# Kernel optimization log

Hardware: AMD Instinct MI355X
Metric: run time of the kernel (lower is better)

## Reference

```python
import jax, jax.numpy as jnp
import numpy as np

S0 = 192
C = [16, 32, 48, 64, 80]      # nPlanes = m*i, m=16, 5 strides
SL = [192, 96, 48, 24, 12]    # spatial size per level
OFF27 = jnp.asarray(np.stack(np.meshgrid(*([[-1, 0, 1]] * 3), indexing='ij'), -1).reshape(-1, 3), jnp.int32)
OFF8 = jnp.asarray(np.stack(np.meshgrid(*([[0, 1]] * 3), indexing='ij'), -1).reshape(-1, 3), jnp.int32)


def _flat(c, S):
    return (c[..., 0] * S + c[..., 1]) * S + c[..., 2]


def _grid(coords, S):
    g = jnp.full((S * S * S,), -1, jnp.int32)
    return g.at[_flat(coords, S)].set(jnp.arange(coords.shape[0], dtype=jnp.int32))


def _subconv(feat, coords, grid, S, W):
    # submanifold 3x3x3 conv over active sites only; W: [27, a, b]
    nb = coords[:, None, :] + OFF27                      # [N,27,3]
    valid = jnp.all((nb >= 0) & (nb < S), axis=-1)
    idx = grid[_flat(jnp.clip(nb, 0, S - 1), S)]         # [N,27]
    valid = valid & (idx >= 0)
    g = jnp.where(valid[..., None], feat[jnp.maximum(idx, 0)], 0.0)
    return jnp.einsum('nka,kab->nb', g, W)


def _downconv(feat, grid_f, S_f, out_coords, W):
    # kernel-2 stride-2 sparse conv; W: [8, a, b]
    src = out_coords[:, None, :] * 2 + OFF8              # [M,8,3]
    valid = jnp.all(src < S_f, axis=-1)
    idx = grid_f[_flat(src, S_f)]
    valid = valid & (idx >= 0)
    g = jnp.where(valid[..., None], feat[jnp.maximum(idx, 0)], 0.0)
    return jnp.einsum('nka,kab->nb', g, W)


def _bnrelu(x, g, b, eps=1e-4):
    # BatchNormLeakyReLU(leakiness=0) == BN (batch stats over active sites) + ReLU
    mu = jnp.mean(x, 0)
    var = jnp.mean((x - mu) ** 2, 0)
    return jax.nn.relu((x - mu) * jax.lax.rsqrt(var + eps) * g + b)


def _unpool(feat_c, grid_c, S_c, fine_coords, k):
    # UnPooling x k levels: copy coarse parent feature to each fine active site
    return feat_c[grid_c[_flat(fine_coords // (1 << k), S_c)]]


def _selection(scores):
    return (jax.nn.softmax(scores, axis=1)[:, 1:2] > 0.5).astype(scores.dtype)


def _forward(coords, features, w_in, blk_w, blk_g, blk_b, dn_g, dn_b, dn_w,
             ppn1_w, ppn1_sw, ppn2_w, ppn2_sw, ppn3_w, ppn3_pw, ppn3_sw):
    grids = [_grid(coords[l], SL[l]) for l in range(5)]
    x = _subconv(features, coords[0], grids[0], SL[0], w_in)   # input layer
    fmaps = [x]
    for i in range(4):  # encoder levels with residual blocks + downsample
        for r in range(2):
            h = _bnrelu(x, blk_g[i][2 * r], blk_b[i][2 * r])
            h = _subconv(h, coords[i], grids[i], SL[i], blk_w[i][2 * r])
            h = _bnrelu(h, blk_g[i][2 * r + 1], blk_b[i][2 * r + 1])
            h = _subconv(h, coords[i], grids[i], SL[i], blk_w[i][2 * r + 1])
            x = x + h  # ConcatTable(Identity, conv path) + AddTable, a==b
        x = _downconv(_bnrelu(x, dn_g[i], dn_b[i]), grids[i], SL[i], coords[i + 1], dn_w[i])
        fmaps.append(x)
    x = _subconv(x, coords[4], grids[4], SL[4], ppn1_w)
    ppn1_scores = x @ ppn1_sw                                   # 1x1 conv
    att1 = _unpool(_selection(ppn1_scores), grids[4], SL[4], coords[2], 2)
    y = fmaps[2] * att1                                         # Multiply at half_stride
    y = _subconv(y, coords[2], grids[2], SL[2], ppn2_w)
    ppn2_scores = y @ ppn2_sw
    att2 = _unpool(_selection(ppn2_scores), grids[2], SL[2], coords[0], 2)
    z = fmaps[0] * att2
    z = _subconv(z, coords[0], grids[0], SL[0], ppn3_w)
    out0 = jnp.concatenate([z @ ppn3_pw, z @ ppn3_sw], axis=1)
    out1 = jnp.concatenate([coords[4].astype(out0.dtype), ppn1_scores], axis=1)
    out2 = jnp.concatenate([coords[2].astype(out0.dtype), ppn2_scores], axis=1)
    return out0, out1, out2


def _make_coords():
    rng = np.random.RandomState(0)
    c0 = np.unique(rng.randint(0, S0, size=(100000, 3)), axis=0).astype(np.int32)
    cs = [c0]
    for _ in range(4):
        cs.append(np.unique(cs[-1] // 2, axis=0).astype(np.int32))
    return cs


def setup_inputs():
    key = jax.random.key(0)
    ks = iter(jax.random.split(key, 64))
    cs = _make_coords()
    inp = {f'coords{l}': jnp.asarray(cs[l]) for l in range(5)}
    N0 = cs[0].shape[0]
    inp['features'] = jax.random.normal(next(ks), (N0, 1), jnp.float32)

    def w(k, shape, fan):
        return jax.random.normal(k, shape, jnp.float32) * (fan ** -0.5)

    inp['w_in'] = w(next(ks), (27, 1, C[0]), 27)
    for i in range(4):
        inp[f'blk_w{i}'] = w(next(ks), (4, 27, C[i], C[i]), 27 * C[i])
        inp[f'blk_g{i}'] = jnp.ones((4, C[i]), jnp.float32)
        inp[f'blk_b{i}'] = jnp.zeros((4, C[i]), jnp.float32)
        inp[f'dn_g{i}'] = jnp.ones((C[i],), jnp.float32)
        inp[f'dn_b{i}'] = jnp.zeros((C[i],), jnp.float32)
        inp[f'dn_w{i}'] = w(next(ks), (8, C[i], C[i + 1]), 8 * C[i])
    inp['ppn1_w'] = w(next(ks), (27, C[4], C[4]), 27 * C[4])
    inp['ppn1_sw'] = w(next(ks), (C[4], 2), C[4])
    inp['ppn2_w'] = w(next(ks), (27, C[2], C[2]), 27 * C[2])
    inp['ppn2_sw'] = w(next(ks), (C[2], 2), C[2])
    inp['ppn3_w'] = w(next(ks), (27, C[0], C[0]), 27 * C[0])
    inp['ppn3_pw'] = w(next(ks), (C[0], 3), C[0])
    inp['ppn3_sw'] = w(next(ks), (C[0], 2), C[0])
    return inp


def reference(features, w_in,
              blk_w0, blk_g0, blk_b0, dn_g0, dn_b0, dn_w0,
              blk_w1, blk_g1, blk_b1, dn_g1, dn_b1, dn_w1,
              blk_w2, blk_g2, blk_b2, dn_g2, dn_b2, dn_w2,
              blk_w3, blk_g3, blk_b3, dn_g3, dn_b3, dn_w3,
              ppn1_w, ppn1_sw, ppn2_w, ppn2_sw, ppn3_w, ppn3_pw, ppn3_sw,
              coords0, coords1, coords2, coords3, coords4):
    coords = [coords0, coords1, coords2, coords3, coords4]
    return _forward(coords, features, w_in,
                    [blk_w0, blk_w1, blk_w2, blk_w3],
                    [blk_g0, blk_g1, blk_g2, blk_g3],
                    [blk_b0, blk_b1, blk_b2, blk_b3],
                    [dn_g0, dn_g1, dn_g2, dn_g3],
                    [dn_b0, dn_b1, dn_b2, dn_b3],
                    [dn_w0, dn_w1, dn_w2, dn_w3],
                    ppn1_w, ppn1_sw, ppn2_w, ppn2_sw, ppn3_w, ppn3_pw, ppn3_sw)
```

## Files before the change

kernel.cpp:

```cpp
#include <hip/hip_runtime.h>
#include <cstdint>
#include <cstddef>

#define TPB 256

typedef _Float16 f16x8 __attribute__((ext_vector_type(8)));
typedef float f32x4 __attribute__((ext_vector_type(4)));


static __global__ void kscatter(int* __restrict__ grid, const int* __restrict__ coords,
                                int N, int S) {
    int i = blockIdx.x * blockDim.x + threadIdx.x;
    if (i >= N) return;
    int x = coords[3 * i], y = coords[3 * i + 1], z = coords[3 * i + 2];
    grid[(x * S + y) * S + z] = i;
}

static __global__ void knbr27(int* __restrict__ nbr, const int* __restrict__ coords,
                              const int* __restrict__ grid, int N, int S, int zr) {
    int t = blockIdx.x * blockDim.x + threadIdx.x;
    if (t >= N * 27) return;
    int n = t / 27, k = t - 27 * n;
    int x = coords[3 * n]     + (k / 9) - 1;
    int y = coords[3 * n + 1] + ((k / 3) % 3) - 1;
    int z = coords[3 * n + 2] + (k % 3) - 1;
    int v = -1;
    if ((unsigned)x < (unsigned)S && (unsigned)y < (unsigned)S && (unsigned)z < (unsigned)S)
        v = grid[(x * S + y) * S + z];
    nbr[t] = (v < 0) ? zr : v;
}

static __global__ void kdown8(int* __restrict__ dn, const int* __restrict__ coords,
                              const int* __restrict__ grid, int M, int S_f, int zr) {
    int t = blockIdx.x * blockDim.x + threadIdx.x;
    if (t >= M * 8) return;
    int n = t >> 3, k = t & 7;
    int x = coords[3 * n] * 2     + ((k >> 2) & 1);
    int y = coords[3 * n + 1] * 2 + ((k >> 1) & 1);
    int z = coords[3 * n + 2] * 2 + (k & 1);
    int v = grid[(x * S_f + y) * S_f + z];
    dn[t] = (v < 0) ? zr : v;
}

static __global__ void kup(int* __restrict__ up, const int* __restrict__ cf,
                           const int* __restrict__ gc, int N, int Sc) {
    int n = blockIdx.x * blockDim.x + threadIdx.x;
    if (n >= N) return;
    int x = cf[3 * n] >> 2, y = cf[3 * n + 1] >> 2, z = cf[3 * n + 2] >> 2;
    up[n] = gc[(x * Sc + y) * Sc + z];
}

static __global__ void ksplitw(_Float16* __restrict__ dst, const float* __restrict__ src,
                               int KREAL, int KPAD, int A, int B) {
    int t = blockIdx.x * blockDim.x + threadIdx.x;
    if (t >= KPAD * A * B) return;
    int a = t % A;
    int b = (t / A) % B;
    int k = t / (A * B);
    float v = (k < KREAL) ? src[((size_t)k * A + a) * B + b] : 0.0f;
    _Float16 hi = (_Float16)v;
    _Float16 lo = (_Float16)(v - (float)hi);
    size_t row = ((size_t)k * B + b) * (size_t)(2 * A);
    dst[row + a] = hi;
    dst[row + A + a] = lo;
}


static __global__ void kstats(double* __restrict__ st, const float* __restrict__ x,
                              int N, int C) {
    extern __shared__ double sh[];
    int tid = threadIdx.x;
    int c = tid % C, rl = tid / C;
    double s = 0.0, q = 0.0;
    int base = blockIdx.x * 256 + rl * 64;
    for (int it = 0; it < 64; it++) {
        int r = base + it;
        if (r < N) {
            double v = (double)x[(size_t)r * C + c];
            s += v;
            q = fma(v, v, q);
        }
    }
    double* ss = sh;
    double* sq = sh + 4 * C;
    ss[tid] = s; sq[tid] = q;
    __syncthreads();
    if (tid < C) {
        double S = ss[tid] + ss[tid + C] + ss[tid + 2 * C] + ss[tid + 3 * C];
        double Q = sq[tid] + sq[tid + C] + sq[tid + 2 * C] + sq[tid + 3 * C];
        atomicAdd(&st[tid], S);
        atomicAdd(&st[80 + tid], Q);
    }
}

static __global__ void kbnrelu_h(_Float16* __restrict__ y, const float4* __restrict__ x,
                                 const double* __restrict__ st, const float* __restrict__ g,
                                 const float* __restrict__ b, int N, int C) {
    __shared__ float sc[80], bh[80];
    int tid = threadIdx.x;
    if (tid < C) {
        double invN = 1.0 / (double)N;
        double S = st[tid] + st[160 + tid] + st[320 + tid] + st[480 + tid];
        double Q = st[80 + tid] + st[240 + tid] + st[400 + tid] + st[560 + tid];
        double mu = S * invN;
        double var = Q * invN - mu * mu;
        float s = g[tid] * rsqrtf((float)var + 1e-4f);
        sc[tid] = s;
        bh[tid] = b[tid] - (float)mu * s;
    }
    __syncthreads();
    int C8 = C >> 3;
    int chunks = (N + 1) * C8;
    int t = blockIdx.x * blockDim.x + tid;
    if (t >= chunks) return;
    int n = t / C8, cc = t - n * C8;
    f16x8 hi = {}, lo = {};
    if (n < N) {
        float4 q0 = x[n * (C >> 2) + cc * 2];
        float4 q1 = x[n * (C >> 2) + cc * 2 + 1];
        float v[8] = {q0.x, q0.y, q0.z, q0.w, q1.x, q1.y, q1.z, q1.w};
#pragma unroll
        for (int j = 0; j < 8; j++) {
            float r = fmaxf(fmaf(v[j], sc[cc * 8 + j], bh[cc * 8 + j]), 0.0f);
            _Float16 h = (_Float16)r;
            hi[j] = h;
            lo[j] = (_Float16)(r - (float)h);
        }
    }
    *(f16x8*)&y[(size_t)n * 2 * C + cc * 8] = hi;
    *(f16x8*)&y[(size_t)n * 2 * C + C + cc * 8] = lo;
}

static __global__ void kcvt_h(_Float16* __restrict__ y, const float4* __restrict__ x,
                              int N, int C) {
    int C8 = C >> 3;
    int t = blockIdx.x * blockDim.x + threadIdx.x;
    if (t >= (N + 1) * C8) return;
    int n = t / C8, cc = t - n * C8;
    f16x8 hi = {}, lo = {};
    if (n < N) {
        float4 q0 = x[n * (C >> 2) + cc * 2];
        float4 q1 = x[n * (C >> 2) + cc * 2 + 1];
        float v[8] = {q0.x, q0.y, q0.z, q0.w, q1.x, q1.y, q1.z, q1.w};
#pragma unroll
        for (int j = 0; j < 8; j++) {
            _Float16 h = (_Float16)v[j];
            hi[j] = h;
            lo[j] = (_Float16)(v[j] - (float)h);
        }
    }
    *(f16x8*)&y[(size_t)n * 2 * C + cc * 8] = hi;
    *(f16x8*)&y[(size_t)n * 2 * C + C + cc * 8] = lo;
}

static __global__ void kmulatt_h(_Float16* __restrict__ y, const float4* __restrict__ fmap,
                                 const int* __restrict__ up, const float* __restrict__ sc,
                                 int N, int C) {
    int C8 = C >> 3;
    int t = blockIdx.x * blockDim.x + threadIdx.x;
    if (t >= (N + 1) * C8) return;
    int n = t / C8, cc = t - n * C8;
    f16x8 hi = {}, lo = {};
    if (n < N) {
        int p = up[n];
        float att = (sc[2 * p + 1] > sc[2 * p]) ? 1.0f : 0.0f;
        float4 q0 = fmap[n * (C >> 2) + cc * 2];
        float4 q1 = fmap[n * (C >> 2) + cc * 2 + 1];
        float v[8] = {q0.x, q0.y, q0.z, q0.w, q1.x, q1.y, q1.z, q1.w};
#pragma unroll
        for (int j = 0; j < 8; j++) {
            float r = v[j] * att;
            _Float16 h = (_Float16)r;
            hi[j] = h;
            lo[j] = (_Float16)(r - (float)h);
        }
    }
    *(f16x8*)&y[(size_t)n * 2 * C + cc * 8] = hi;
    *(f16x8*)&y[(size_t)n * 2 * C + C + cc * 8] = lo;
}


template <int A, int B, int TAPS, int TPI, int TR, int MT, int KG, bool ADD>
__launch_bounds__(256, 3)
static __global__ void kconvmf(float* __restrict__ out, const _Float16* __restrict__ feat,
                               const int* __restrict__ nbr, const _Float16* __restrict__ Wsp,
                               const float* __restrict__ res, double* __restrict__ stp,
                               int N, int zr) {
    constexpr int NT_W = B / 16;
    static_assert(TR == 4 * MT * 16, "tile/wave mismatch");
    constexpr int KPT = (TPI == 1) ? ((A + 31) & ~31)
                      : (TPI == 2) ? ((A + 15) & ~15)
                                   : ((A + 7) & ~7);
    constexpr int KT = TPI * KPT;
    static_assert(KT % 32 == 0, "KT must be multiple of 32");
    constexpr int KSTEPS = KT / 32;
    constexpr int KTCH = KT / 8;
    constexpr int PKT = (KTCH == 12) ? 16 : KTCH;
    static_assert(PKT == 8 || PKT == 16, "bad PKT");
    constexpr int RH = PKT * 8;
    constexpr int QQ = KPT / 8;
    constexpr int AQ = A / 8;
    constexpr int A2 = 2 * A;
    constexpr int ITERS = (TAPS + TPI - 1) / TPI;
    constexpr int IPG = (ITERS + KG - 1) / KG;
    constexpr int WROWS = 2 * B;
    constexpr int WSBH = WROWS * RH;
    constexpr int WTOT = WROWS * KTCH;
    constexpr int WPT = (WTOT + 255) / 256;

    __shared__ __attribute__((aligned(16))) _Float16 wsb[2 * WSBH];

    const int tid = threadIdx.x;

    int bx;
    {
        int nwg = gridDim.x, bid = blockIdx.x;
        int q = nwg >> 3, r = nwg & 7, xcd = bid & 7, ix = bid >> 3;
        bx = (xcd < r) ? xcd * (q + 1) + ix : r * (q + 1) + (xcd - r) * q + ix;
    }
    const int row0 = bx * TR;
    const int it0 = (KG > 1) ? blockIdx.y * IPG : 0;
    const int it1 = (KG > 1) ? ((it0 + IPG < ITERS) ? it0 + IPG : ITERS) : ITERS;

    const int lane = tid & 63, wid = tid >> 6;
    const int lrow = lane & 15, lgrp = lane >> 4;
    const int mb = wid * MT * 16;

    int w_lds[WPT], w_off[WPT];
    bool w_ok[WPT], w_real[WPT];
#pragma unroll
    for (int i = 0; i < WPT; i++) {
        int task = tid + i * 256;
        bool ok = (WTOT % 256 == 0) || (task < WTOT);
        int tc = ok ? task : 0;
        int q = tc % KTCH;
        int row = tc / KTCH;
        int bcol = row % B, pp = row / B;
        int t = q / QQ, qq = q - t * QQ;
        w_lds[i] = row * RH + (q ^ (row & (PKT - 1))) * 8;
        w_off[i] = (t * B + bcol) * A2 + pp * A + qq * 8;
        w_ok[i] = ok;
        w_real[i] = ok && (qq < AQ);
    }
    int rowm[MT];
#pragma unroll
    for (int mt = 0; mt < MT; mt++) rowm[mt] = row0 + mb + mt * 16 + lrow;

    f32x4 acc[MT][NT_W];
#pragma unroll
    for (int mt = 0; mt < MT; mt++)
#pragma unroll
        for (int nt = 0; nt < NT_W; nt++)
            acc[mt][nt] = (f32x4){0.f, 0.f, 0.f, 0.f};

    int nidA[MT][TPI], nidB[MT][TPI];
    f16x8 faA[MT][KSTEPS][2], faB[MT][KSTEPS][2];
    f16x8 wg[WPT];

    auto loadnbr = [&](auto& nd, int it) {
        int tb = it * TPI;
#pragma unroll
        for (int mt = 0; mt < MT; mt++)
#pragma unroll
            for (int t = 0; t < TPI; t++)
                nd[mt][t] = (rowm[mt] < N && tb + t < TAPS)
                          ? nbr[(size_t)rowm[mt] * TAPS + tb + t] : zr;
    };
    auto loadA = [&](auto& fd, const auto& nd) {
#pragma unroll
        for (int mt = 0; mt < MT; mt++)
#pragma unroll
            for (int ks = 0; ks < KSTEPS; ks++) {
                int qc = ks * 4 + lgrp;
                int t = qc / QQ;
                int cq = qc - t * QQ;
                int id;
                if constexpr (TPI == 1) id = nd[mt][0];
                else if constexpr (TPI == 2) id = (t == 0) ? nd[mt][0] : nd[mt][1];
                else {
                    int lo2 = (t == 0) ? nd[mt][0] : nd[mt][1];
                    int hi2 = (t == 2) ? nd[mt][2] : nd[mt][3];
                    id = (t < 2) ? lo2 : hi2;
                }
                const _Float16* p = feat + (size_t)id * A2 + cq * 8;
                if constexpr (QQ > AQ) {
                    bool okc = (cq < AQ);
                    fd[mt][ks][0] = okc ? *(const f16x8*)p : (f16x8){};
                    fd[mt][ks][1] = okc ? *(const f16x8*)(p + A) : (f16x8){};
                } else {
                    fd[mt][ks][0] = *(const f16x8*)p;
                    fd[mt][ks][1] = *(const f16x8*)(p + A);
                }
            }
    };
    auto loadW = [&](int it) {
        size_t base = (size_t)it * TPI * B * A2;
#pragma unroll
        for (int i = 0; i < WPT; i++)
            wg[i] = w_real[i] ? *(const f16x8*)&Wsp[base + w_off[i]] : (f16x8){};
    };
    auto storeW = [&](int c) {
        _Float16* d = wsb + c * WSBH;
#pragma unroll
        for (int i = 0; i < WPT; i++)
            if (w_ok[i]) *(f16x8*)&d[w_lds[i]] = wg[i];
    };
    auto domfma = [&](const auto& fd, int cb) {
#pragma unroll
        for (int ks = 0; ks < KSTEPS; ++ks) {
            const int qc = ks * 4 + lgrp;
            f16x8 bh[NT_W], bl[NT_W];
#pragma unroll
            for (int nt = 0; nt < NT_W; ++nt) {
                int rH = nt * 16 + lrow;
                bh[nt] = *(const f16x8*)&wsb[cb + rH * RH + (qc ^ (rH & (PKT - 1))) * 8];
                int rL = B + rH;
                bl[nt] = *(const f16x8*)&wsb[cb + rL * RH + (qc ^ (rL & (PKT - 1))) * 8];
            }
#pragma unroll
            for (int mt = 0; mt < MT; ++mt)
#pragma unroll
                for (int nt = 0; nt < NT_W; ++nt) {
                    acc[mt][nt] = __builtin_amdgcn_mfma_f32_16x16x32_f16(fd[mt][ks][0], bh[nt], acc[mt][nt], 0, 0, 0);
                    acc[mt][nt] = __builtin_amdgcn_mfma_f32_16x16x32_f16(fd[mt][ks][1], bh[nt], acc[mt][nt], 0, 0, 0);
                    acc[mt][nt] = __builtin_amdgcn_mfma_f32_16x16x32_f16(fd[mt][ks][0], bl[nt], acc[mt][nt], 0, 0, 0);
                }
        }
    };

    loadnbr(nidA, it0);
    loadA(faA, nidA);
    loadW(it0);
    storeW(0);
    if (it0 + 1 < it1) loadnbr(nidB, it0 + 1);
    __syncthreads();
    if (it0 + 1 < it1) loadW(it0 + 1);

    int cur = 0;
    auto body = [&](const auto& fc, auto& fn, auto& nc, const auto& nn, int it) {
        const bool m1 = (it + 1 < it1), m2 = (it + 2 < it1);
        if (m1) {
            storeW(cur ^ 1);
            loadA(fn, nn);
        }
        if (m2) loadnbr(nc, it + 2);
        domfma(fc, cur * WSBH);
        if (m2) loadW(it + 2);
        if (m1) __syncthreads();
        cur ^= 1;
    };
    for (int it = it0; it < it1; ) {
        body(faA, faB, nidA, nidB, it); ++it;
        if (it >= it1) break;
        body(faB, faA, nidB, nidA, it); ++it;
    }

    const bool dostats = (stp != nullptr);
    double ssum[NT_W], sqs[NT_W];
#pragma unroll
    for (int nt = 0; nt < NT_W; nt++) { ssum[nt] = 0.0; sqs[nt] = 0.0; }
#pragma unroll
    for (int mt = 0; mt < MT; ++mt) {
        int gr0 = row0 + mb + mt * 16 + lgrp * 4;
#pragma unroll
        for (int nt = 0; nt < NT_W; ++nt) {
            int gc = nt * 16 + lrow;
#pragma unroll
            for (int j = 0; j < 4; ++j) {
                int r = gr0 + j;
                if (r < N) {
                    size_t o = (size_t)r * B + gc;
                    if (KG > 1) {
                        atomicAdd(&out[o], acc[mt][nt][j]);
                    } else {
                        float v = acc[mt][nt][j];
                        if (ADD) v += res[o];
                        out[o] = v;
                        if (dostats) {
                            double dv = (double)v;
                            ssum[nt] += dv;
                            sqs[nt] = fma(dv, dv, sqs[nt]);
                        }
                    }
                }
            }
        }
    }
    if (KG == 1 && dostats) {
#pragma unroll
        for (int nt = 0; nt < NT_W; nt++) {
            ssum[nt] += __shfl_xor(ssum[nt], 16, 64);
            ssum[nt] += __shfl_xor(ssum[nt], 32, 64);
            sqs[nt] += __shfl_xor(sqs[nt], 16, 64);
            sqs[nt] += __shfl_xor(sqs[nt], 32, 64);
        }
        if (lgrp == 0) {
            double* sb = stp + ((bx + wid) & 3) * 160;
#pragma unroll
            for (int nt = 0; nt < NT_W; nt++) {
                int gc = nt * 16 + lrow;
                atomicAdd(&sb[gc], ssum[nt]);
                atomicAdd(&sb[80 + gc], sqs[nt]);
            }
        }
    }
}

static __global__ void kconv_in(float* __restrict__ out, const float* __restrict__ f,
                                const int* __restrict__ nbr, const float* __restrict__ W,
                                int N, int zr) {
    int t = blockIdx.x * blockDim.x + threadIdx.x;
    if (t >= N * 4) return;
    int n = t >> 2, bq = t & 3;
    float4 acc = make_float4(0.f, 0.f, 0.f, 0.f);
    const float4* W4 = (const float4*)W;
    for (int k = 0; k < 27; k++) {
        int id = nbr[n * 27 + k];
        if (id == zr) continue;
        float v = f[id];
        float4 w = W4[k * 4 + bq];
        acc.x = fmaf(v, w.x, acc.x);
        acc.y = fmaf(v, w.y, acc.y);
        acc.z = fmaf(v, w.z, acc.z);
        acc.w = fmaf(v, w.w, acc.w);
    }
    ((float4*)out)[n * 4 + bq] = acc;
}


static __global__ void kscores(float* __restrict__ sc, const float* __restrict__ x,
                               const float* __restrict__ w, int N, int C) {
    int n = blockIdx.x * blockDim.x + threadIdx.x;
    if (n >= N) return;
    float s0 = 0.0f, s1 = 0.0f;
    const float* xr = x + (size_t)n * C;
    for (int c = 0; c < C; c++) {
        float v = xr[c];
        s0 = fmaf(v, w[2 * c], s0);
        s1 = fmaf(v, w[2 * c + 1], s1);
    }
    sc[2 * n] = s0;
    sc[2 * n + 1] = s1;
}

static __global__ void kout0(float* __restrict__ out, const float* __restrict__ z,
                             const float* __restrict__ pw, const float* __restrict__ sw,
                             int N) {
    int n = blockIdx.x * blockDim.x + threadIdx.x;
    if (n >= N) return;
    float o0 = 0, o1 = 0, o2 = 0, o3 = 0, o4 = 0;
    const float* zr = z + (size_t)n * 16;
#pragma unroll
    for (int c = 0; c < 16; c++) {
        float v = zr[c];
        o0 = fmaf(v, pw[3 * c], o0);
        o1 = fmaf(v, pw[3 * c + 1], o1);
        o2 = fmaf(v, pw[3 * c + 2], o2);
        o3 = fmaf(v, sw[2 * c], o3);
        o4 = fmaf(v, sw[2 * c + 1], o4);
    }
    float* r = out + (size_t)n * 5;
    r[0] = o0; r[1] = o1; r[2] = o2; r[3] = o3; r[4] = o4;
}

static __global__ void koutc(float* __restrict__ out, const int* __restrict__ coords,
                             const float* __restrict__ sc, int N) {
    int n = blockIdx.x * blockDim.x + threadIdx.x;
    if (n >= N) return;
    float* r = out + (size_t)n * 5;
    r[0] = (float)coords[3 * n];
    r[1] = (float)coords[3 * n + 1];
    r[2] = (float)coords[3 * n + 2];
    r[3] = sc[2 * n];
    r[4] = sc[2 * n + 1];
}


static inline int cdiv(long a, int b) { return (int)((a + b - 1) / b); }

static void conv(hipStream_t s, float* out, const _Float16* feat, const int* nbr,
                 const _Float16* Wsp, const float* res, double* stp,
                 int N, int A, int B, int TAPS, int zr) {
#define CASE(AA, BB, TT, TPI_, TR_, MT_, KG_)                                              \
    else if (A == AA && B == BB && TAPS == TT) {                                           \
        if (KG_ > 1 && !res) hipMemsetAsync(out, 0, (size_t)N * BB * 4, s);                \
        dim3 g(cdiv(N, TR_), KG_), blk(256);                                               \
        if (res) kconvmf<AA, BB, TT, TPI_, TR_, MT_, KG_, true><<<g, blk, 0, s>>>(out, feat, nbr, Wsp, res, stp, N, zr); \
        else     kconvmf<AA, BB, TT, TPI_, TR_, MT_, KG_, false><<<g, blk, 0, s>>>(out, feat, nbr, Wsp, nullptr, stp, N, zr); \
    }
    if (false) {}
    CASE(16, 16, 27,  4, 128,  2, 1)
    CASE(32, 32, 27,  2,  64,  1, 1)
    CASE(48, 48, 27,  2,  64,  1, 1)
    CASE(64, 64, 27,  1,  64,  1, 4)
    CASE(80, 80, 27,  1,  64,  1, 9)
    CASE(16, 32,  8,  4, 128,  2, 1)
    CASE(32, 48,  8,  2,  64,  1, 1)
    CASE(48, 64,  8,  2,  64,  1, 2)
    CASE(64, 80,  8,  1,  64,  1, 8)
#undef CASE
}

static void bnapply(hipStream_t s, _Float16* out, const float* x, double* st,
                    const float* g, const float* b, int N, int C, bool pre) {
    if (!pre)
        kstats<<<cdiv(N, 256), 4 * C, 8 * C * 2 * sizeof(double), s>>>(st, x, N, C);
    int chunks = (N + 1) * (C / 8);
    kbnrelu_h<<<cdiv(chunks, 256), 256, 0, s>>>(out, (const float4*)x, st, g, b, N, C);
}

extern "C" void kernel_launch(void* const* d_in, const int* in_sizes, int n_in,
                              void* d_out, int out_size, void* d_ws, size_t ws_size,
                              hipStream_t stream) {
    (void)n_in; (void)out_size; (void)ws_size;
    const int SL[5] = {192, 96, 48, 24, 12};
    const int C[5] = {16, 32, 48, 64, 80};
    int N[5];
    const int* coords[5];
    for (int l = 0; l < 5; l++) { N[l] = in_sizes[l] / 3; coords[l] = (const int*)d_in[l]; }
    const float* features = (const float*)d_in[5];
    const float* w_in = (const float*)d_in[6];
    const float *blk_w[4], *blk_g[4], *blk_b[4], *dn_g[4], *dn_b[4], *dn_w[4];
    for (int i = 0; i < 4; i++) {
        blk_w[i] = (const float*)d_in[7 + 6 * i];
        blk_g[i] = (const float*)d_in[8 + 6 * i];
        blk_b[i] = (const float*)d_in[9 + 6 * i];
        dn_g[i] = (const float*)d_in[10 + 6 * i];
        dn_b[i] = (const float*)d_in[11 + 6 * i];
        dn_w[i] = (const float*)d_in[12 + 6 * i];
    }
    const float* ppn1_w  = (const float*)d_in[31];
    const float* ppn1_sw = (const float*)d_in[32];
    const float* ppn2_w  = (const float*)d_in[33];
    const float* ppn2_sw = (const float*)d_in[34];
    const float* ppn3_w  = (const float*)d_in[35];
    const float* ppn3_pw = (const float*)d_in[36];
    const float* ppn3_sw = (const float*)d_in[37];
    float* dout = (float*)d_out;

    char* ws = (char*)d_ws;
    size_t off = 0;
    auto alloc = [&](size_t bytes) -> char* {
        off = (off + 255) & ~(size_t)255;
        char* p = ws + off;
        off += bytes;
        return p;
    };
    int* nbr[5];
    for (int l = 0; l < 5; l++) nbr[l] = (int*)alloc((size_t)N[l] * 27 * 4);
    int* down8[4];
    for (int i = 0; i < 4; i++) down8[i] = (int*)alloc((size_t)N[i + 1] * 8 * 4);
    int* up1 = (int*)alloc((size_t)N[2] * 4);
    int* up2 = (int*)alloc((size_t)N[0] * 4);
    double* stats = (double*)alloc(26 * 640 * sizeof(double));
    _Float16* blkWsp[4];
    _Float16* dnWsp[4];
    for (int i = 0; i < 4; i++) {
        blkWsp[i] = (_Float16*)alloc((size_t)4 * 28 * C[i] * 2 * C[i] * 2);
        dnWsp[i] = (_Float16*)alloc((size_t)8 * C[i + 1] * 2 * C[i] * 2);
    }
    _Float16* p1Wsp = (_Float16*)alloc((size_t)27 * 80 * 160 * 2);
    _Float16* p2Wsp = (_Float16*)alloc((size_t)28 * 48 * 96 * 2);
    _Float16* p3Wsp = (_Float16*)alloc((size_t)28 * 16 * 32 * 2);
    float* fmap0 = (float*)alloc((size_t)N[0] * 16 * 4);
    float* fmap2 = (float*)alloc((size_t)N[2] * 48 * 4);
    float* sc1 = (float*)alloc((size_t)N[4] * 2 * 4);
    float* sc2 = (float*)alloc((size_t)N[2] * 2 * 4);

    size_t BIG = 0;
    for (int l = 0; l < 5; l++) {
        size_t s = (size_t)(N[l] + 1) * C[l] * 4;
        if (s > BIG) BIG = s;
    }
    BIG = (BIG + 255) & ~(size_t)255;
    off = (off + 255) & ~(size_t)255;
    size_t trans = off;
    int* grid[5];
    size_t gtot = 0;
    for (int l = 0; l < 5; l++) {
        grid[l] = (int*)(ws + trans + gtot);
        gtot += (size_t)SL[l] * SL[l] * SL[l] * 4;
    }
    float* B0 = (float*)(ws + trans);
    float* B1 = (float*)(ws + trans + BIG);
    float* B2 = (float*)(ws + trans + 2 * BIG);

    hipMemsetAsync(ws + trans, 0xFF, gtot, stream);
    hipMemsetAsync(stats, 0, 26 * 640 * sizeof(double), stream);
    for (int l = 0; l < 5; l++)
        kscatter<<<cdiv(N[l], TPB), TPB, 0, stream>>>(grid[l], coords[l], N[l], SL[l]);
    for (int l = 0; l < 5; l++)
        knbr27<<<cdiv((long)N[l] * 27, TPB), TPB, 0, stream>>>(nbr[l], coords[l], grid[l], N[l], SL[l], N[l]);
    for (int i = 0; i < 4; i++)
        kdown8<<<cdiv((long)N[i + 1] * 8, TPB), TPB, 0, stream>>>(down8[i], coords[i + 1], grid[i], N[i + 1], SL[i], N[i]);
    kup<<<cdiv(N[2], TPB), TPB, 0, stream>>>(up1, coords[2], grid[4], N[2], 12);
    kup<<<cdiv(N[0], TPB), TPB, 0, stream>>>(up2, coords[0], grid[2], N[0], 48);
    for (int i = 0; i < 4; i++) {
        int Ci = C[i];
        for (int c = 0; c < 4; c++) {
            int n1 = 28 * Ci * Ci;
            ksplitw<<<cdiv(n1, TPB), TPB, 0, stream>>>(
                blkWsp[i] + (size_t)c * 28 * Ci * 2 * Ci,
                blk_w[i] + (size_t)c * 27 * Ci * Ci, 27, 28, Ci, Ci);
        }
        int n2 = 8 * Ci * C[i + 1];
        ksplitw<<<cdiv(n2, TPB), TPB, 0, stream>>>(dnWsp[i], dn_w[i], 8, 8, Ci, C[i + 1]);
    }
    ksplitw<<<cdiv(27 * 6400, TPB), TPB, 0, stream>>>(p1Wsp, ppn1_w, 27, 27, 80, 80);
    ksplitw<<<cdiv(28 * 2304, TPB), TPB, 0, stream>>>(p2Wsp, ppn2_w, 27, 28, 48, 48);
    ksplitw<<<cdiv(28 * 256, TPB), TPB, 0, stream>>>(p3Wsp, ppn3_w, 27, 28, 16, 16);

    int slot = 0;
    auto stn = [&]() { return stats + 640 * (slot++); };
    auto stpeek = [&]() { return stats + 640 * slot; };

    float* curX = B0;
    kconv_in<<<cdiv((long)N[0] * 4, TPB), TPB, 0, stream>>>(curX, features, nbr[0], w_in, N[0], N[0]);
    hipMemcpyAsync(fmap0, curX, (size_t)N[0] * 16 * 4, hipMemcpyDeviceToDevice, stream);

    auto others = [&](float* cur, float*& t1, float*& t2) {
        if (cur == B0) { t1 = B1; t2 = B2; }
        else if (cur == B1) { t1 = B0; t2 = B2; }
        else { t1 = B0; t2 = B1; }
    };

    bool entryPre = false;
    for (int i = 0; i < 4; i++) {
        int Ni = N[i], Ci = C[i];
        float *T1, *T2;
        others(curX, T1, T2);
        size_t wsl = (size_t)28 * Ci * 2 * Ci;
        bool fuseL = (i < 3);
        for (int r = 0; r < 2; r++) {
            bnapply(stream, (_Float16*)T1, curX, stn(), blk_g[i] + (2 * r) * Ci,
                    blk_b[i] + (2 * r) * Ci, Ni, Ci, r == 0 ? entryPre : fuseL);
            conv(stream, T2, (const _Float16*)T1, nbr[i], blkWsp[i] + (2 * r) * wsl,
                 nullptr, fuseL ? stpeek() : nullptr, Ni, Ci, Ci, 27, Ni);
            bnapply(stream, (_Float16*)T1, T2, stn(), blk_g[i] + (2 * r + 1) * Ci,
                    blk_b[i] + (2 * r + 1) * Ci, Ni, Ci, fuseL);
            conv(stream, curX, (const _Float16*)T1, nbr[i], blkWsp[i] + (2 * r + 1) * wsl,
                 curX, fuseL ? stpeek() : nullptr, Ni, Ci, Ci, 27, Ni);
        }
        bnapply(stream, (_Float16*)T1, curX, stn(), dn_g[i], dn_b[i], Ni, Ci, fuseL);
        bool fuseD = (i < 2);
        conv(stream, T2, (const _Float16*)T1, down8[i], dnWsp[i], nullptr,
             fuseD ? stpeek() : nullptr, N[i + 1], Ci, C[i + 1], 8, Ni);
        entryPre = fuseD;
        if (i == 1)
            hipMemcpyAsync(fmap2, T2, (size_t)N[2] * 48 * 4, hipMemcpyDeviceToDevice, stream);
        curX = T2;
    }

    float *T1, *T2;
    others(curX, T1, T2);
    kcvt_h<<<cdiv((N[4] + 1) * 10, TPB), TPB, 0, stream>>>((_Float16*)T1, (const float4*)curX, N[4], 80);
    conv(stream, T2, (const _Float16*)T1, nbr[4], p1Wsp, nullptr, nullptr, N[4], 80, 80, 27, N[4]);
    kscores<<<cdiv(N[4], TPB), TPB, 0, stream>>>(sc1, T2, ppn1_sw, N[4], 80);
    koutc<<<cdiv(N[4], TPB), TPB, 0, stream>>>(dout + (size_t)N[0] * 5, coords[4], sc1, N[4]);
    kmulatt_h<<<cdiv((long)(N[2] + 1) * 6, TPB), TPB, 0, stream>>>((_Float16*)curX, (const float4*)fmap2, up1, sc1, N[2], 48);
    conv(stream, T1, (const _Float16*)curX, nbr[2], p2Wsp, nullptr, nullptr, N[2], 48, 48, 27, N[2]);
    kscores<<<cdiv(N[2], TPB), TPB, 0, stream>>>(sc2, T1, ppn2_sw, N[2], 48);
    koutc<<<cdiv(N[2], TPB), TPB, 0, stream>>>(dout + (size_t)(N[0] + N[4]) * 5, coords[2], sc2, N[2]);
    kmulatt_h<<<cdiv((long)(N[0] + 1) * 2, TPB), TPB, 0, stream>>>((_Float16*)T2, (const float4*)fmap0, up2, sc2, N[0], 16);
    conv(stream, curX, (const _Float16*)T2, nbr[0], p3Wsp, nullptr, nullptr, N[0], 16, 16, 27, N[0]);
    kout0<<<cdiv(N[0], TPB), TPB, 0, stream>>>(dout, curX, ppn3_pw, ppn3_sw, N[0]);
}
```

Before: 1.404 ms.

## Enlarge conv row tiles, add block-level stats reduction, lighten barriers

Several conv configurations move from 64-row to 128-row tiles with two m-tiles per wave, and launch bounds drop from 3 to 2 waves per SIMD to leave room for the extra registers. BN statistics are now reduced across the four waves in shared memory, and one wave issues the atomics into 16 spread slots instead of 4, which cuts atomic contention. Stats buffers grow to match, and the bnrelu kernel sums 16 partials. Plain __syncthreads is replaced by an explicit LDS waitcnt plus s_barrier, which trims the wait on outstanding global loads but means correctness depends on the barrier only needing LDS ordering.

```diff
diff --git a/kernel.cpp b/kernel.cpp
--- a/kernel.cpp
+++ b/kernel.cpp
@@ -6,6 +6,13 @@
 
 typedef _Float16 f16x8 __attribute__((ext_vector_type(8)));
 typedef float f32x4 __attribute__((ext_vector_type(4)));
+
+__device__ __forceinline__ void block_sync_lds() {
+    asm volatile("s_waitcnt lgkmcnt(0)" ::: "memory");
+    __builtin_amdgcn_sched_barrier(0);
+    __builtin_amdgcn_s_barrier();
+    __builtin_amdgcn_sched_barrier(0);
+}
 
 
 static __global__ void kscatter(int* __restrict__ grid, const int* __restrict__ coords,
@@ -100,8 +107,12 @@
     int tid = threadIdx.x;
     if (tid < C) {
         double invN = 1.0 / (double)N;
-        double S = st[tid] + st[160 + tid] + st[320 + tid] + st[480 + tid];
-        double Q = st[80 + tid] + st[240 + tid] + st[400 + tid] + st[560 + tid];
+        double S = 0.0, Q = 0.0;
+#pragma unroll
+        for (int c = 0; c < 16; c++) {
+            S += st[c * 160 + tid];
+            Q += st[c * 160 + 80 + tid];
+        }
         double mu = S * invN;
         double var = Q * invN - mu * mu;
         float s = g[tid] * rsqrtf((float)var + 1e-4f);
@@ -181,7 +192,7 @@
 
 
 template <int A, int B, int TAPS, int TPI, int TR, int MT, int KG, bool ADD>
-__launch_bounds__(256, 3)
+__launch_bounds__(256, 2)
 static __global__ void kconvmf(float* __restrict__ out, const _Float16* __restrict__ feat,
                                const int* __restrict__ nbr, const _Float16* __restrict__ Wsp,
                                const float* __restrict__ res, double* __restrict__ stp,
@@ -209,6 +220,7 @@
     constexpr int WPT = (WTOT + 255) / 256;
 
     __shared__ __attribute__((aligned(16))) _Float16 wsb[2 * WSBH];
+    __shared__ double sred[(KG == 1) ? 4 * 2 * B : 1];
 
     const int tid = threadIdx.x;
 
@@ -333,7 +345,7 @@
     loadW(it0);
     storeW(0);
     if (it0 + 1 < it1) loadnbr(nidB, it0 + 1);
-    __syncthreads();
+    block_sync_lds();
     if (it0 + 1 < it1) loadW(it0 + 1);
 
     int cur = 0;
@@ -346,7 +358,7 @@
         if (m2) loadnbr(nc, it + 2);
         domfma(fc, cur * WSBH);
         if (m2) loadW(it + 2);
-        if (m1) __syncthreads();
+        if (m1) block_sync_lds();
         cur ^= 1;
     };
     for (int it = it0; it < it1; ) {
@@ -386,21 +398,31 @@
             }
         }
     }
-    if (KG == 1 && dostats) {
-#pragma unroll
-        for (int nt = 0; nt < NT_W; nt++) {
-            ssum[nt] += __shfl_xor(ssum[nt], 16, 64);
-            ssum[nt] += __shfl_xor(ssum[nt], 32, 64);
-            sqs[nt] += __shfl_xor(sqs[nt], 16, 64);
-            sqs[nt] += __shfl_xor(sqs[nt], 32, 64);
-        }
-        if (lgrp == 0) {
-            double* sb = stp + ((bx + wid) & 3) * 160;
+    if (KG == 1) {
+        if (dostats) {
 #pragma unroll
             for (int nt = 0; nt < NT_W; nt++) {
-                int gc = nt * 16 + lrow;
-                atomicAdd(&sb[gc], ssum[nt]);
-                atomicAdd(&sb[80 + gc], sqs[nt]);
+                ssum[nt] += __shfl_xor(ssum[nt], 16, 64);
+                ssum[nt] += __shfl_xor(ssum[nt], 32, 64);
+                sqs[nt] += __shfl_xor(sqs[nt], 16, 64);
+                sqs[nt] += __shfl_xor(sqs[nt], 32, 64);
+            }
+            if (lgrp == 0) {
+#pragma unroll
+                for (int nt = 0; nt < NT_W; nt++) {
+                    sred[(wid * 2 + 0) * B + nt * 16 + lrow] = ssum[nt];
+                    sred[(wid * 2 + 1) * B + nt * 16 + lrow] = sqs[nt];
+                }
+            }
+            __syncthreads();
+            if (wid == 0) {
+                double* sb = stp + (bx & 15) * 160;
+                for (int c = lane; c < B; c += 64) {
+                    double S = sred[c] + sred[2 * B + c] + sred[4 * B + c] + sred[6 * B + c];
+                    double Q = sred[B + c] + sred[3 * B + c] + sred[5 * B + c] + sred[7 * B + c];
+                    atomicAdd(&sb[c], S);
+                    atomicAdd(&sb[80 + c], Q);
+                }
             }
         }
     }
@@ -490,12 +512,12 @@
     }
     if (false) {}
     CASE(16, 16, 27,  4, 128,  2, 1)
-    CASE(32, 32, 27,  2,  64,  1, 1)
-    CASE(48, 48, 27,  2,  64,  1, 1)
-    CASE(64, 64, 27,  1,  64,  1, 4)
+    CASE(32, 32, 27,  2, 128,  2, 1)
+    CASE(48, 48, 27,  2, 128,  2, 1)
+    CASE(64, 64, 27,  1, 128,  2, 4)
     CASE(80, 80, 27,  1,  64,  1, 9)
     CASE(16, 32,  8,  4, 128,  2, 1)
-    CASE(32, 48,  8,  2,  64,  1, 1)
+    CASE(32, 48,  8,  2, 128,  2, 1)
     CASE(48, 64,  8,  2,  64,  1, 2)
     CASE(64, 80,  8,  1,  64,  1, 8)
 #undef CASE
@@ -552,7 +574,7 @@
     for (int i = 0; i < 4; i++) down8[i] = (int*)alloc((size_t)N[i + 1] * 8 * 4);
     int* up1 = (int*)alloc((size_t)N[2] * 4);
     int* up2 = (int*)alloc((size_t)N[0] * 4);
-    double* stats = (double*)alloc(26 * 640 * sizeof(double));
+    double* stats = (double*)alloc((size_t)26 * 2560 * sizeof(double));
     _Float16* blkWsp[4];
     _Float16* dnWsp[4];
     for (int i = 0; i < 4; i++) {
@@ -586,7 +608,7 @@
     float* B2 = (float*)(ws + trans + 2 * BIG);
 
     hipMemsetAsync(ws + trans, 0xFF, gtot, stream);
-    hipMemsetAsync(stats, 0, 26 * 640 * sizeof(double), stream);
+    hipMemsetAsync(stats, 0, (size_t)26 * 2560 * sizeof(double), stream);
     for (int l = 0; l < 5; l++)
         kscatter<<<cdiv(N[l], TPB), TPB, 0, stream>>>(grid[l], coords[l], N[l], SL[l]);
     for (int l = 0; l < 5; l++)
@@ -611,8 +633,8 @@
     ksplitw<<<cdiv(28 * 256, TPB), TPB, 0, stream>>>(p3Wsp, ppn3_w, 27, 28, 16, 16);
 
     int slot = 0;
-    auto stn = [&]() { return stats + 640 * (slot++); };
-    auto stpeek = [&]() { return stats + 640 * slot; };
+    auto stn = [&]() { return stats + 2560 * (slot++); };
+    auto stpeek = [&]() { return stats + 2560 * slot; };
 
     float* curX = B0;
     kconv_in<<<cdiv((long)N[0] * 4, TPB), TPB, 0, stream>>>(curX, features, nbr[0], w_in, N[0], N[0]);
```

New measurement: 1.288 ms. -8.3%, faster.
